# Kernel optimization log

Hardware: AMD Instinct MI355X
Metric: run time of the kernel (lower is better)

The kernel has to match this reference:

```python
import jax, jax.numpy as jnp
import numpy as np

N_NODES = 50000
N_EDGES = 600000
IN_CH, HID_CH, OUT_CH = 128, 128, 64
N_GRAPHS = 64


def glorot(key, shape):
    fan_in, fan_out = shape
    lim = np.sqrt(6.0 / (fan_in + fan_out)).astype(np.float32)
    return jax.random.uniform(key, shape, jnp.float32, -lim, lim)


def setup_inputs() -> dict:
    key = jax.random.key(0)
    k1, k2, k3, k4, k5 = jax.random.split(key, 5)
    x = jax.random.normal(k1, (N_NODES, IN_CH), jnp.float32)
    edge_index = jax.random.randint(k2, (2, N_EDGES), 0, N_NODES, jnp.int64)
    batch = jnp.sort(jax.random.randint(k3, (N_NODES,), 0, N_GRAPHS, jnp.int64))
    W1 = glorot(k4, (IN_CH, HID_CH))
    b1 = jnp.zeros((HID_CH,), jnp.float32)
    W2 = glorot(k5, (HID_CH, OUT_CH))
    b2 = jnp.zeros((OUT_CH,), jnp.float32)
    return {"x": x, "edge_index": edge_index, "batch": batch,
            "W1": W1, "b1": b1, "W2": W2, "b2": b2}


def gcn_conv(x, edge_index, W, b):
    # PyG GCNConv: x' = D^-1/2 (A + I) D^-1/2 (x W) + b
    h = x @ W                                   # [N, F_out]
    loop = jnp.arange(N_NODES, dtype=edge_index.dtype)
    src = jnp.concatenate([edge_index[0], loop])  # [E+N]
    dst = jnp.concatenate([edge_index[1], loop])
    deg = jax.ops.segment_sum(jnp.ones_like(dst, h.dtype), dst,
                              num_segments=N_NODES)
    dinv = jnp.where(deg > 0, jax.lax.rsqrt(deg), 0.0)
    norm = dinv[src] * dinv[dst]                # [E+N]
    msg = h[src] * norm[:, None]                # gather + per-edge scale
    out = jax.ops.segment_sum(msg, dst, num_segments=N_NODES)  # scatter-add
    return out + b


def reference(x, edge_index, batch, W1, b1, W2, b2):
    h = jax.nn.relu(gcn_conv(x, edge_index, W1, b1))
    h = gcn_conv(h, edge_index, W2, b2)
    # global_add_pool: segment-sum of node features by graph id
    return jax.ops.segment_sum(h, batch, num_segments=N_GRAPHS)  # [G, OUT]
```

## Files before the change

kernel.cpp:

```cpp
#include <hip/hip_runtime.h>

#define NNODES 50000
#define NEDGES 600000
#define NGRAPHS 64
#define NBKT 196
#define EB 293
#define CHK 2048
#define GEMM_BLKS 196

typedef __attribute__((ext_vector_type(8))) short short8;
typedef __attribute__((ext_vector_type(4))) float f32x4;

__device__ inline short f2bf(float f) {
    unsigned u = __float_as_uint(f);
    u = (u + 0x7fffu + ((u >> 16) & 1u)) >> 16;
    return (short)u;
}
__device__ inline float bf2f(unsigned short s) {
    return __uint_as_float(((unsigned)s) << 16);
}
__device__ inline float bf_lo(unsigned w) { return __uint_as_float(w << 16); }
__device__ inline float bf_hi(unsigned w) { return __uint_as_float(w & 0xffff0000u); }
__device__ inline void fmabf8(const uint4 m, float n, float* a) {
    a[0] = fmaf(bf_lo(m.x), n, a[0]); a[1] = fmaf(bf_hi(m.x), n, a[1]);
    a[2] = fmaf(bf_lo(m.y), n, a[2]); a[3] = fmaf(bf_hi(m.y), n, a[3]);
    a[4] = fmaf(bf_lo(m.z), n, a[4]); a[5] = fmaf(bf_hi(m.z), n, a[5]);
    a[6] = fmaf(bf_lo(m.w), n, a[6]); a[7] = fmaf(bf_hi(m.w), n, a[7]);
}
__device__ inline void addbf8(const uint4 m, float* a) {
    a[0] += bf_lo(m.x); a[1] += bf_hi(m.x);
    a[2] += bf_lo(m.y); a[3] += bf_hi(m.y);
    a[4] += bf_lo(m.z); a[5] += bf_hi(m.z);
    a[6] += bf_lo(m.w); a[7] += bf_hi(m.w);
}

__device__ inline uint4 make_frag(const float* __restrict__ W, int M, int idx) {
    int lane = idx & 63, ks = (idx >> 6) & 3, cf = idx >> 8;
    int c = cf * 16 + (lane & 15);
    int k0 = ks * 32 + (lane >> 4) * 8;
    unsigned t[8];
    #pragma unroll
    for (int j = 0; j < 8; ++j)
        t[j] = (unsigned short)f2bf(W[(k0 + j) * M + c]);
    uint4 o;
    o.x = t[0] | (t[1] << 16);
    o.y = t[2] | (t[3] << 16);
    o.z = t[4] | (t[5] << 16);
    o.w = t[6] | (t[7] << 16);
    return o;
}

__global__ __launch_bounds__(256) void k_init0(const float* __restrict__ W1,
                                               const float* __restrict__ W2,
                                               unsigned short* __restrict__ Wf1,
                                               unsigned short* __restrict__ Wf2,
                                               float* __restrict__ dout) {
    int idx = blockIdx.x * 256 + threadIdx.x;
    if (idx < NGRAPHS * 64) dout[idx] = 0.f;
    if (idx < 2048) {
        ((uint4*)Wf1)[idx] = make_frag(W1, 128, idx);
    } else if (idx < 3072) {
        ((uint4*)Wf2)[idx - 2048] = make_frag(W2, 64, idx - 2048);
    }
}

__global__ __launch_bounds__(256) void k_mega1(const float* __restrict__ X,
                                               const unsigned short* __restrict__ Wf,
                                               unsigned short* __restrict__ Y,
                                               const int* __restrict__ ei,
                                               int* __restrict__ bh) {
    constexpr int CF = 8;
    constexpr int SLOTS = CF * 4 * 64;
    __shared__ uint4 Bl[SLOTS];
    __shared__ int hist[NBKT];
    const int tid = threadIdx.x;

    if (blockIdx.x >= GEMM_BLKS) {
        int eb = blockIdx.x - GEMM_BLKS;
        for (int i = tid; i < NBKT; i += 256) hist[i] = 0;
        __syncthreads();
        int e0 = eb * CHK;
        int e1 = min(e0 + CHK, NEDGES);
        for (int i = e0 + tid; i < e1; i += 256)
            atomicAdd(&hist[ei[NEDGES + i] >> 8], 1);
        __syncthreads();
        for (int i = tid; i < NBKT; i += 256) bh[i * EB + eb] = hist[i];
        return;
    }

    for (int i = tid; i < SLOTS; i += 256) Bl[i] = ((const uint4*)Wf)[i];
    __syncthreads();

    const short8* Bs8 = (const short8*)Bl;
    const int lane = tid & 63;
    const int wave = tid >> 6;
    const int qr = lane >> 4;
    const int cl = lane & 15;
    const int wid = blockIdx.x * 4 + wave;
    const int ngroups = (NNODES + 63) / 64;
    if (wid >= ngroups) return;

    const int base = wid * 64;
    short8 a[4][4];
    #pragma unroll
    for (int r = 0; r < 4; ++r) {
        int arow = base + r * 16 + cl;
        bool ok = arow < NNODES;
        #pragma unroll
        for (int ks = 0; ks < 4; ++ks) {
            short8 v = (short8)0;
            if (ok) {
                const float* xp = X + (long)arow * 128 + ks * 32 + qr * 8;
                float4 x0 = *reinterpret_cast<const float4*>(xp);
                float4 x1 = *reinterpret_cast<const float4*>(xp + 4);
                v[0] = f2bf(x0.x); v[1] = f2bf(x0.y); v[2] = f2bf(x0.z); v[3] = f2bf(x0.w);
                v[4] = f2bf(x1.x); v[5] = f2bf(x1.y); v[6] = f2bf(x1.z); v[7] = f2bf(x1.w);
            }
            a[r][ks] = v;
        }
    }
    f32x4 acc[4][CF];
    #pragma unroll
    for (int r = 0; r < 4; ++r)
        #pragma unroll
        for (int cf = 0; cf < CF; ++cf)
            acc[r][cf] = (f32x4){0.f, 0.f, 0.f, 0.f};
    #pragma unroll
    for (int cf = 0; cf < CF; ++cf)
        #pragma unroll
        for (int ks = 0; ks < 4; ++ks) {
            short8 b = Bs8[(cf * 4 + ks) * 64 + lane];
            #pragma unroll
            for (int r = 0; r < 4; ++r)
                acc[r][cf] = __builtin_amdgcn_mfma_f32_16x16x32_bf16(a[r][ks], b, acc[r][cf], 0, 0, 0);
        }
    #pragma unroll
    for (int r = 0; r < 4; ++r) {
        int row0 = base + r * 16 + qr * 4;
        #pragma unroll
        for (int i = 0; i < 4; ++i) {
            int row = row0 + i;
            if (row < NNODES) {
                #pragma unroll
                for (int cf = 0; cf < CF; ++cf)
                    Y[(long)row * 128 + cf * 16 + cl] = (unsigned short)f2bf(acc[r][cf][i]);
            }
        }
    }
}

__global__ __launch_bounds__(512) void k_scanA1(int* __restrict__ bh,
                                                int* __restrict__ bt) {
    __shared__ int s[512];
    int b = blockIdx.x;
    int t = threadIdx.x;
    int v = (t < EB) ? bh[b * EB + t] : 0;
    s[t] = v;
    __syncthreads();
    for (int off = 1; off < 512; off <<= 1) {
        int u = (t >= off) ? s[t - off] : 0;
        __syncthreads();
        s[t] += u;
        __syncthreads();
    }
    if (t < EB) bh[b * EB + t] = s[t] - v;
    if (t == EB - 1) bt[b] = s[t];
}

__global__ __launch_bounds__(256) void k_scanA2(int* __restrict__ bt) {
    __shared__ int s[256];
    int t = threadIdx.x;
    int v = (t < NBKT) ? bt[t] : 0;
    s[t] = v;
    __syncthreads();
    for (int off = 1; off < 256; off <<= 1) {
        int u = (t >= off) ? s[t - off] : 0;
        __syncthreads();
        s[t] += u;
        __syncthreads();
    }
    if (t < NBKT) bt[t] = s[t] - v;
}

__global__ __launch_bounds__(256) void k_passA2(const int* __restrict__ ei,
                                                const int* __restrict__ bh,
                                                const int* __restrict__ bt,
                                                int2* __restrict__ parted) {
    __shared__ int cur[NBKT];
    int eb = blockIdx.x;
    int tid = threadIdx.x;
    for (int i = tid; i < NBKT; i += 256) cur[i] = bt[i] + bh[i * EB + eb];
    __syncthreads();
    int e0 = eb * CHK;
    int e1 = min(e0 + CHK, NEDGES);
    for (int i = e0 + tid; i < e1; i += 256) {
        int s = ei[i];
        int d = ei[NEDGES + i];
        int pos = atomicAdd(&cur[d >> 8], 1);
        parted[pos] = make_int2(s, d);
    }
}

__global__ __launch_bounds__(256) void k_passB(const int* __restrict__ bt,
                                               const int2* __restrict__ parted,
                                               int* __restrict__ rp,
                                               int* __restrict__ csr,
                                               float* __restrict__ dinv) {
    __shared__ int cnt2[256], cur[256], sc[256];
    int b = blockIdx.x;
    int t = threadIdx.x;
    cnt2[t] = 0;
    __syncthreads();
    int lo = bt[b];
    int hi = (b == NBKT - 1) ? NEDGES : bt[b + 1];
    for (int i = lo + t; i < hi; i += 256)
        atomicAdd(&cnt2[parted[i].y & 255], 1);
    __syncthreads();
    sc[t] = cnt2[t];
    __syncthreads();
    for (int o = 1; o < 256; o <<= 1) {
        int u = (t >= o) ? sc[t - o] : 0;
        __syncthreads();
        sc[t] += u;
        __syncthreads();
    }
    int excl = sc[t] - cnt2[t];
    cur[t] = excl;
    int v = b * 256 + t;
    if (v < NNODES) {
        rp[v] = lo + excl;
        dinv[v] = rsqrtf((float)cnt2[t] + 1.0f);
    } else if (v == NNODES) {
        rp[v] = lo + excl;
    }
    __syncthreads();
    for (int i = lo + t; i < hi; i += 256) {
        int2 e = parted[i];
        int pos = lo + atomicAdd(&cur[e.y & 255], 1);
        csr[pos] = e.x;
    }
}

__global__ __launch_bounds__(256) void k_gather_gemm(const int* __restrict__ rp,
                                                     const int* __restrict__ csr_src,
                                                     const float* __restrict__ dinv,
                                                     const unsigned short* __restrict__ Hs,
                                                     const float* __restrict__ b1,
                                                     const unsigned short* __restrict__ Wf2,
                                                     unsigned short* __restrict__ Y) {
    __shared__ uint4 Bl[1024];
    __shared__ unsigned short h1[64 * 128];
    const int tid = threadIdx.x;
    const int lane = tid & 63;
    const int wave = tid >> 6;
    for (int i = tid; i < 1024; i += 256) Bl[i] = ((const uint4*)Wf2)[i];

    const int grp = lane >> 4;
    const int ln = lane & 15;
    const int c8 = ln * 8;
    const int base = blockIdx.x * 64;
    const uint4* Hp = (const uint4*)Hs;
    float4 bv0 = *reinterpret_cast<const float4*>(b1 + c8);
    float4 bv1 = *reinterpret_cast<const float4*>(b1 + c8 + 4);
    float bb[8] = {bv0.x, bv0.y, bv0.z, bv0.w, bv1.x, bv1.y, bv1.z, bv1.w};

    #pragma unroll
    for (int p = 0; p < 4; ++p) {
        int vloc = wave * 16 + p * 4 + grp;
        int v = base + vloc;
        uint4 o = {0u, 0u, 0u, 0u};
        if (v < NNODES) {
            float a[8] = {0, 0, 0, 0, 0, 0, 0, 0};
            float dd = dinv[v];
            fmabf8(Hp[((long)v * 128 + c8) >> 3], dd, a);
            int lo = rp[v], hi = rp[v + 1];
            int i = lo;
            for (; i + 4 <= hi; i += 4) {
                int s0 = csr_src[i], s1 = csr_src[i + 1];
                int s2 = csr_src[i + 2], s3 = csr_src[i + 3];
                float n0 = dinv[s0], n1 = dinv[s1], n2 = dinv[s2], n3 = dinv[s3];
                uint4 m0 = Hp[((long)s0 * 128 + c8) >> 3];
                uint4 m1 = Hp[((long)s1 * 128 + c8) >> 3];
                uint4 m2 = Hp[((long)s2 * 128 + c8) >> 3];
                uint4 m3 = Hp[((long)s3 * 128 + c8) >> 3];
                fmabf8(m0, n0, a); fmabf8(m1, n1, a);
                fmabf8(m2, n2, a); fmabf8(m3, n3, a);
            }
            for (; i < hi; ++i) {
                int s = csr_src[i];
                fmabf8(Hp[((long)s * 128 + c8) >> 3], dinv[s], a);
            }
            unsigned t[8];
            #pragma unroll
            for (int j = 0; j < 8; ++j) {
                float y = fmaxf(fmaf(a[j], dd, bb[j]), 0.f);
                t[j] = (unsigned short)f2bf(y);
            }
            o.x = t[0] | (t[1] << 16);
            o.y = t[2] | (t[3] << 16);
            o.z = t[4] | (t[5] << 16);
            o.w = t[6] | (t[7] << 16);
        }
        int byte = (vloc * 256 + c8 * 2) ^ ((vloc & 7) << 4);
        *reinterpret_cast<uint4*>((char*)h1 + byte) = o;
    }
    __syncthreads();

    const int qr = lane >> 4;
    const int cl = lane & 15;
    const int arow = wave * 16 + cl;
    short8 afr[4];
    #pragma unroll
    for (int ks = 0; ks < 4; ++ks) {
        int byte = (arow * 256 + (ks * 32 + qr * 8) * 2) ^ ((arow & 7) << 4);
        afr[ks] = *reinterpret_cast<const short8*>((const char*)h1 + byte);
    }
    const short8* Bs8 = (const short8*)Bl;
    f32x4 acc[4];
    #pragma unroll
    for (int cf = 0; cf < 4; ++cf) acc[cf] = (f32x4){0.f, 0.f, 0.f, 0.f};
    #pragma unroll
    for (int cf = 0; cf < 4; ++cf)
        #pragma unroll
        for (int ks = 0; ks < 4; ++ks)
            acc[cf] = __builtin_amdgcn_mfma_f32_16x16x32_bf16(afr[ks], Bs8[(cf * 4 + ks) * 64 + lane], acc[cf], 0, 0, 0);
    #pragma unroll
    for (int i = 0; i < 4; ++i) {
        int row = base + wave * 16 + qr * 4 + i;
        if (row < NNODES) {
            float dv = dinv[row];
            #pragma unroll
            for (int cf = 0; cf < 4; ++cf)
                Y[(long)row * 64 + cf * 16 + cl] = (unsigned short)f2bf(acc[cf][i] * dv);
        }
    }
}

__global__ __launch_bounds__(256) void k_gather2(const int* __restrict__ rp,
                                                 const int* __restrict__ csr_src,
                                                 const float* __restrict__ dinv,
                                                 const unsigned short* __restrict__ Hs,
                                                 const float* __restrict__ bias,
                                                 unsigned short* __restrict__ out) {
    int lane = threadIdx.x & 7;
    int grp = threadIdx.x >> 3;
    int v = blockIdx.x * 32 + grp;
    if (v >= NNODES) return;
    int c8 = lane * 8;
    float dd = dinv[v];
    float a[8] = {0, 0, 0, 0, 0, 0, 0, 0};
    const uint4* Hp = (const uint4*)Hs;
    addbf8(Hp[((long)v * 64 + c8) >> 3], a);
    int lo = rp[v], hi = rp[v + 1];
    int i = lo;
    for (; i + 4 <= hi; i += 4) {
        int s0 = csr_src[i], s1 = csr_src[i + 1], s2 = csr_src[i + 2], s3 = csr_src[i + 3];
        uint4 m0 = Hp[((long)s0 * 64 + c8) >> 3];
        uint4 m1 = Hp[((long)s1 * 64 + c8) >> 3];
        uint4 m2 = Hp[((long)s2 * 64 + c8) >> 3];
        uint4 m3 = Hp[((long)s3 * 64 + c8) >> 3];
        addbf8(m0, a); addbf8(m1, a); addbf8(m2, a); addbf8(m3, a);
    }
    for (; i < hi; ++i)
        addbf8(Hp[((long)csr_src[i] * 64 + c8) >> 3], a);
    unsigned t[8];
    #pragma unroll
    for (int j = 0; j < 8; ++j)
        t[j] = (unsigned short)f2bf(fmaf(a[j], dd, bias[c8 + j]));
    uint4 o;
    o.x = t[0] | (t[1] << 16);
    o.y = t[2] | (t[3] << 16);
    o.z = t[4] | (t[5] << 16);
    o.w = t[6] | (t[7] << 16);
    ((uint4*)out)[((long)v * 64 + c8) >> 3] = o;
}

__device__ inline int lower_bound_i(const int* a, int n, int key) {
    int lo = 0, hi = n;
    while (lo < hi) {
        int mid = (lo + hi) >> 1;
        if (a[mid] < key) lo = mid + 1; else hi = mid;
    }
    return lo;
}

__global__ __launch_bounds__(256) void k_pool(const unsigned short* __restrict__ h2,
                                              const int* __restrict__ batch,
                                              float* __restrict__ out) {
    int g = blockIdx.x >> 4;
    int slice = blockIdx.x & 15;
    int lo = lower_bound_i(batch, NNODES, g);
    int hi = lower_bound_i(batch, NNODES, g + 1);
    int ch = threadIdx.x & 63;
    int part = threadIdx.x >> 6;
    float acc = 0.f;
    for (int v = lo + slice * 4 + part; v < hi; v += 64)
        acc += bf2f(h2[(long)v * 64 + ch]);
    __shared__ float red[256];
    red[threadIdx.x] = acc;
    __syncthreads();
    if (part == 0) {
        float s = red[ch] + red[64 + ch] + red[128 + ch] + red[192 + ch];
        atomicAdd(&out[g * 64 + ch], s);
    }
}

extern "C" void kernel_launch(void* const* d_in, const int* in_sizes, int n_in,
                              void* d_out, int out_size, void* d_ws, size_t ws_size,
                              hipStream_t stream) {
    const float* x   = (const float*)d_in[0];
    const int* ei    = (const int*)d_in[1];
    const int* batch = (const int*)d_in[2];
    const float* W1  = (const float*)d_in[3];
    const float* b1  = (const float*)d_in[4];
    const float* W2  = (const float*)d_in[5];
    const float* b2  = (const float*)d_in[6];
    float* out = (float*)d_out;

    char* ws = (char*)d_ws;
    float* dinv = (float*)ws;
    int*   rp   = (int*)(ws + (256 << 10));
    int*   bh   = (int*)(ws + (512 << 10));
    int*   bt   = (int*)(ws + (768 << 10));
    int*   csr  = (int*)(ws + (1u << 20));
    unsigned short* Wf1 = (unsigned short*)(ws + (3584u << 10));
    unsigned short* Wf2 = (unsigned short*)(ws + (3584u << 10) + (32 << 10));
    unsigned short* bufA = (unsigned short*)(ws + (4u << 20));
    unsigned short* bufB = (unsigned short*)(ws + (4u << 20) + (size_t)NNODES * 128 * 2);
    int2* parted = (int2*)bufB;

    k_init0<<<16, 256, 0, stream>>>(W1, W2, Wf1, Wf2, out);

    k_mega1<<<GEMM_BLKS + EB, 256, 0, stream>>>(x, Wf1, bufA, ei, bh);

    k_scanA1<<<NBKT, 512, 0, stream>>>(bh, bt);
    k_scanA2<<<1, 256, 0, stream>>>(bt);

    k_passA2<<<EB, 256, 0, stream>>>(ei, bh, bt, parted);
    k_passB<<<NBKT, 256, 0, stream>>>(bt, parted, rp, csr, dinv);

    k_gather_gemm<<<(NNODES + 63) / 64, 256, 0, stream>>>(rp, csr, dinv, bufA, b1, Wf2, bufB);

    k_gather2<<<(NNODES + 31) / 32, 256, 0, stream>>>(rp, csr, dinv, bufB, b2, bufA);

    k_pool<<<NGRAPHS * 16, 256, 0, stream>>>(bufA, batch, out);
}
```

Measured before the change: 100.3 us.

## Fold bucket-total scan into consumers, vectorize edge loads, read W2 from global

Removes the single-block k_scanA2 launch and instead has every block of k_passA2 and k_passB redo the 196-entry prefix scan of bucket totals in shared memory. This drops one serialized launch from the chain at the cost of some redundant per-block work. The edge histogram and partition loops now read indices as int4, with four atomics per iteration. The second-layer GEMM reads its B fragments straight from global/L2 instead of staging W2 in LDS, which saves LDS and a load phase but risks slower B accesses. The int4 loops assume each edge chunk length is a multiple of 4, which holds for 2048-edge chunks and a final chunk of 1952 edges.

```diff
diff --git a/kernel.cpp b/kernel.cpp
--- a/kernel.cpp
+++ b/kernel.cpp
@@ -81,8 +81,15 @@
         __syncthreads();
         int e0 = eb * CHK;
         int e1 = min(e0 + CHK, NEDGES);
-        for (int i = e0 + tid; i < e1; i += 256)
-            atomicAdd(&hist[ei[NEDGES + i] >> 8], 1);
+        int n4 = (e1 - e0) >> 2;
+        const int4* dp = (const int4*)(ei + NEDGES + e0);
+        for (int i = tid; i < n4; i += 256) {
+            int4 d = dp[i];
+            atomicAdd(&hist[d.x >> 8], 1);
+            atomicAdd(&hist[d.y >> 8], 1);
+            atomicAdd(&hist[d.z >> 8], 1);
+            atomicAdd(&hist[d.w >> 8], 1);
+        }
         __syncthreads();
         for (int i = tid; i < NBKT; i += 256) bh[i * EB + eb] = hist[i];
         return;
@@ -167,37 +174,37 @@
     if (t == EB - 1) bt[b] = s[t];
 }
 
-__global__ __launch_bounds__(256) void k_scanA2(int* __restrict__ bt) {
-    __shared__ int s[256];
-    int t = threadIdx.x;
-    int v = (t < NBKT) ? bt[t] : 0;
-    s[t] = v;
-    __syncthreads();
-    for (int off = 1; off < 256; off <<= 1) {
-        int u = (t >= off) ? s[t - off] : 0;
-        __syncthreads();
-        s[t] += u;
-        __syncthreads();
-    }
-    if (t < NBKT) bt[t] = s[t] - v;
-}
-
 __global__ __launch_bounds__(256) void k_passA2(const int* __restrict__ ei,
                                                 const int* __restrict__ bh,
                                                 const int* __restrict__ bt,
                                                 int2* __restrict__ parted) {
+    __shared__ int sc[256];
     __shared__ int cur[NBKT];
     int eb = blockIdx.x;
-    int tid = threadIdx.x;
-    for (int i = tid; i < NBKT; i += 256) cur[i] = bt[i] + bh[i * EB + eb];
+    int t = threadIdx.x;
+    int v = (t < NBKT) ? bt[t] : 0;
+    sc[t] = v;
+    __syncthreads();
+    for (int off = 1; off < 256; off <<= 1) {
+        int u = (t >= off) ? sc[t - off] : 0;
+        __syncthreads();
+        sc[t] += u;
+        __syncthreads();
+    }
+    if (t < NBKT) cur[t] = (sc[t] - v) + bh[t * EB + eb];
     __syncthreads();
     int e0 = eb * CHK;
     int e1 = min(e0 + CHK, NEDGES);
-    for (int i = e0 + tid; i < e1; i += 256) {
-        int s = ei[i];
-        int d = ei[NEDGES + i];
-        int pos = atomicAdd(&cur[d >> 8], 1);
-        parted[pos] = make_int2(s, d);
+    int n4 = (e1 - e0) >> 2;
+    const int4* sp = (const int4*)(ei + e0);
+    const int4* dp = (const int4*)(ei + NEDGES + e0);
+    for (int i = t; i < n4; i += 256) {
+        int4 sv = sp[i];
+        int4 dv = dp[i];
+        int p0 = atomicAdd(&cur[dv.x >> 8], 1); parted[p0] = make_int2(sv.x, dv.x);
+        int p1 = atomicAdd(&cur[dv.y >> 8], 1); parted[p1] = make_int2(sv.y, dv.y);
+        int p2 = atomicAdd(&cur[dv.z >> 8], 1); parted[p2] = make_int2(sv.z, dv.z);
+        int p3 = atomicAdd(&cur[dv.w >> 8], 1); parted[p3] = make_int2(sv.w, dv.w);
     }
 }
 
@@ -209,10 +216,21 @@
     __shared__ int cnt2[256], cur[256], sc[256];
     int b = blockIdx.x;
     int t = threadIdx.x;
+    int v = (t < NBKT) ? bt[t] : 0;
+    sc[t] = v;
+    __syncthreads();
+    for (int o = 1; o < 256; o <<= 1) {
+        int u = (t >= o) ? sc[t - o] : 0;
+        __syncthreads();
+        sc[t] += u;
+        __syncthreads();
+    }
+    __shared__ int lo_sh, hi_sh;
+    if (t == b) { lo_sh = sc[t] - v; hi_sh = sc[t]; }
+    __syncthreads();
+    int lo = lo_sh, hi = hi_sh;
     cnt2[t] = 0;
     __syncthreads();
-    int lo = bt[b];
-    int hi = (b == NBKT - 1) ? NEDGES : bt[b + 1];
     for (int i = lo + t; i < hi; i += 256)
         atomicAdd(&cnt2[parted[i].y & 255], 1);
     __syncthreads();
@@ -226,12 +244,12 @@
     }
     int excl = sc[t] - cnt2[t];
     cur[t] = excl;
-    int v = b * 256 + t;
-    if (v < NNODES) {
-        rp[v] = lo + excl;
-        dinv[v] = rsqrtf((float)cnt2[t] + 1.0f);
-    } else if (v == NNODES) {
-        rp[v] = lo + excl;
+    int vtx = b * 256 + t;
+    if (vtx < NNODES) {
+        rp[vtx] = lo + excl;
+        dinv[vtx] = rsqrtf((float)cnt2[t] + 1.0f);
+    } else if (vtx == NNODES) {
+        rp[vtx] = lo + excl;
     }
     __syncthreads();
     for (int i = lo + t; i < hi; i += 256) {
@@ -248,12 +266,10 @@
                                                      const float* __restrict__ b1,
                                                      const unsigned short* __restrict__ Wf2,
                                                      unsigned short* __restrict__ Y) {
-    __shared__ uint4 Bl[1024];
     __shared__ unsigned short h1[64 * 128];
     const int tid = threadIdx.x;
     const int lane = tid & 63;
     const int wave = tid >> 6;
-    for (int i = tid; i < 1024; i += 256) Bl[i] = ((const uint4*)Wf2)[i];
 
     const int grp = lane >> 4;
     const int ln = lane & 15;
@@ -315,7 +331,7 @@
         int byte = (arow * 256 + (ks * 32 + qr * 8) * 2) ^ ((arow & 7) << 4);
         afr[ks] = *reinterpret_cast<const short8*>((const char*)h1 + byte);
     }
-    const short8* Bs8 = (const short8*)Bl;
+    const short8* Bs8 = (const short8*)Wf2;
     f32x4 acc[4];
     #pragma unroll
     for (int cf = 0; cf < 4; ++cf) acc[cf] = (f32x4){0.f, 0.f, 0.f, 0.f};
@@ -434,7 +450,6 @@
     k_mega1<<<GEMM_BLKS + EB, 256, 0, stream>>>(x, Wf1, bufA, ei, bh);
 
     k_scanA1<<<NBKT, 512, 0, stream>>>(bh, bt);
-    k_scanA2<<<1, 256, 0, stream>>>(bt);
 
     k_passA2<<<EB, 256, 0, stream>>>(ei, bh, bt, parted);
     k_passB<<<NBKT, 256, 0, stream>>>(bt, parted, rp, csr, dinv);
```

Measured after the change: 98.18 us. 1.02x faster.
